# Kernel optimization log

Hardware: AMD Instinct MI355X
Metric: run time of the kernel (lower is better)

## Reference

```python
import jax, jax.numpy as jnp
import numpy as np

N_NODES = 100000
N_EDGES = 1600000
D_IN = 256
N_HEADS = 4
D_OUT = 32
NEG_SLOPE = 0.2


def setup_inputs() -> dict:
    key = jax.random.key(0)
    k1, k2, k3, k4, k5, k6 = jax.random.split(key, 6)
    x = jax.random.normal(k1, (N_NODES, D_IN), dtype=jnp.float32)
    fc_w = jax.random.normal(k2, (N_HEADS * D_OUT, D_IN), dtype=jnp.float32) * (1.0 / np.sqrt(D_IN))
    attn_l = jax.random.normal(k3, (N_HEADS, D_OUT), dtype=jnp.float32) * 0.1
    attn_r = jax.random.normal(k4, (N_HEADS, D_OUT), dtype=jnp.float32) * 0.1
    src = jax.random.randint(k5, (N_EDGES,), 0, N_NODES, dtype=jnp.int64)
    dst = jax.random.randint(k6, (N_EDGES,), 0, N_NODES, dtype=jnp.int64)
    return {"x": x, "fc_w": fc_w, "attn_l": attn_l, "attn_r": attn_r, "src": src, "dst": dst}


def reference(x, fc_w, attn_l, attn_r, src, dst):
    N = x.shape[0]
    H, F = attn_l.shape
    # Linear projection: ft = fc(x) viewed as [N, H, F]
    ft = (x @ fc_w.T).reshape(N, H, F)
    # Per-node attention logits: el = <ft, a_l>, er = <ft, a_r>  -> [N, H]
    el = jnp.einsum("nhf,hf->nh", ft, attn_l)
    er = jnp.einsum("nhf,hf->nh", ft, attn_r)
    # Edge scores: e = leaky_relu(el[src] + er[dst])  -> [E, H]
    e = el[src] + er[dst]
    e = jnp.where(e > 0, e, NEG_SLOPE * e)
    # Segment (per-destination-node) softmax over incoming edges
    m = jax.ops.segment_max(e, dst, num_segments=N)  # [N, H]
    ex = jnp.exp(e - m[dst])                          # [E, H]
    denom = jax.ops.segment_sum(ex, dst, num_segments=N)  # [N, H]
    a = ex / denom[dst]                               # [E, H]
    # Weighted scatter-sum aggregation: out[n] = sum_{e: dst=n} a_e * ft[src_e]
    out = jax.ops.segment_sum(ft[src] * a[:, :, None], dst, num_segments=N)  # [N, H, F]
    return out
```

## Files before the change

### kernel.cpp

```cpp
#include <hip/hip_runtime.h>
#include <math.h>

#define N_NODES 100000
#define N_EDGES 1600000
#define D_IN 256
#define N_HEADS 4
#define D_OUT 32
#define D_HID 128
#define NEG_SLOPE 0.2f

#define BUCKET_SHIFT 8
#define BUCKET_NODES 256
#define NB ((N_NODES + BUCKET_NODES - 1) / BUCKET_NODES)
#define CAP 6144
#define TILE 2048
#define EPT 8
#define N_TILES ((N_EDGES + TILE - 1) / TILE)

typedef __attribute__((ext_vector_type(8))) short bf16x8;
typedef __attribute__((ext_vector_type(4))) float f32x4;

static __device__ __forceinline__ unsigned cvt2(float lo, float hi) {
  unsigned r;
  asm("v_cvt_pk_bf16_f32 %0, %1, %2" : "=v"(r) : "v"(lo), "v"(hi));
  return r;
}
static __device__ __forceinline__ float bfu_lo(unsigned u) {
  union { unsigned u; float f; } c; c.u = u << 16; return c.f;
}
static __device__ __forceinline__ float bfu_hi(unsigned u) {
  union { unsigned u; float f; } c; c.u = u & 0xFFFF0000u; return c.f;
}

__global__ __launch_bounds__(256) void k_wcvt(const float* __restrict__ w,
                                              unsigned short* __restrict__ wb) {
  int i = blockIdx.x * 256 + threadIdx.x;
  if (i < (D_HID * D_IN) / 4) {
    float4 v = ((const float4*)w)[i];
    ((uint2*)wb)[i] = make_uint2(cvt2(v.x, v.y), cvt2(v.z, v.w));
  }
}

__global__ __launch_bounds__(256, 1) void k_gemm(const float* __restrict__ x,
                                                 const unsigned short* __restrict__ wb,
                                                 const float* __restrict__ al,
                                                 const float* __restrict__ ar,
                                                 unsigned short* __restrict__ ftb,
                                                 float* __restrict__ el,
                                                 float* __restrict__ er) {
  __shared__ char lds[131072];
  char* As = lds;
  char* Ws = lds + 65536;
  int t = threadIdx.x;
  int wave = t >> 6, lane = t & 63;
  int quad = lane >> 4, l16 = lane & 15;
  int rowBlk = blockIdx.x * 128;

  {
    int r = t >> 1, h = t & 1;
    int grow = rowBlk + r;
    bool v = grow < N_NODES;
    const float* xp = x + (size_t)(v ? grow : 0) * D_IN + h * 128;
    unsigned swz = (unsigned)((r & 7) << 4);
    char* abase = As + r * 512 + h * 256;
    char* wbase = Ws + r * 512 + h * 256;
    const uint4* wp = (const uint4*)wb + t * 16;
    const float4 z4 = make_float4(0.f, 0.f, 0.f, 0.f);
    #pragma unroll
    for (int c = 0; c < 16; ++c) {
      float4 v0 = v ? *(const float4*)(xp + c * 8) : z4;
      float4 v1 = v ? *(const float4*)(xp + c * 8 + 4) : z4;
      uint4 wv = wp[c];
      uint4 av = make_uint4(cvt2(v0.x, v0.y), cvt2(v0.z, v0.w),
                            cvt2(v1.x, v1.y), cvt2(v1.z, v1.w));
      *(uint4*)(abase + ((unsigned)(c * 16) ^ swz)) = av;
      *(uint4*)(wbase + ((unsigned)(c * 16) ^ swz)) = wv;
    }
  }
  __syncthreads();

  f32x4 acc[2][8];
  #pragma unroll
  for (int mt = 0; mt < 2; ++mt)
    #pragma unroll
    for (int nt = 0; nt < 8; ++nt) {
      acc[mt][nt][0] = 0.f; acc[mt][nt][1] = 0.f;
      acc[mt][nt][2] = 0.f; acc[mt][nt][3] = 0.f;
    }
  unsigned swzL = (unsigned)((l16 & 7) << 4);
  int m0 = wave * 32 + l16;
  #pragma unroll
  for (int kb = 0; kb < 8; ++kb) {
    unsigned ko = (unsigned)(kb * 64 + quad * 16);
    bf16x8 a0 = *(const bf16x8*)(As + m0 * 512 + (ko ^ swzL));
    bf16x8 a1 = *(const bf16x8*)(As + (m0 + 16) * 512 + (ko ^ swzL));
    bf16x8 b[8];
    #pragma unroll
    for (int nt = 0; nt < 8; ++nt)
      b[nt] = *(const bf16x8*)(Ws + (nt * 16 + l16) * 512 + (ko ^ swzL));
    #pragma unroll
    for (int nt = 0; nt < 8; ++nt) {
      acc[0][nt] = __builtin_amdgcn_mfma_f32_16x16x32_bf16(a0, b[nt], acc[0][nt], 0, 0, 0);
      acc[1][nt] = __builtin_amdgcn_mfma_f32_16x16x32_bf16(a1, b[nt], acc[1][nt], 0, 0, 0);
    }
  }

  int rowBase = rowBlk + wave * 32;

  #pragma unroll
  for (int mt = 0; mt < 2; ++mt) {
    #pragma unroll
    for (int nt = 0; nt < 8; ++nt) {
      int col = nt * 16 + l16;
      #pragma unroll
      for (int r = 0; r < 4; r += 2) {
        unsigned p = cvt2(acc[mt][nt][r], acc[mt][nt][r + 1]);
        int row = rowBase + mt * 16 + quad * 4 + r;
        if (row < N_NODES)
          ftb[(size_t)row * D_HID + col] = (unsigned short)p;
        if (row + 1 < N_NODES)
          ftb[(size_t)(row + 1) * D_HID + col] = (unsigned short)(p >> 16);
      }
    }
  }

  float alf[8], arf[8];
  #pragma unroll
  for (int nt = 0; nt < 8; ++nt) {
    alf[nt] = al[nt * 16 + l16];
    arf[nt] = ar[nt * 16 + l16];
  }
  #pragma unroll
  for (int mt = 0; mt < 2; ++mt) {
    #pragma unroll
    for (int r = 0; r < 4; ++r) {
      int row = rowBase + mt * 16 + quad * 4 + r;
      float sl[4], sr[4];
      #pragma unroll
      for (int h = 0; h < 4; ++h) {
        sl[h] = acc[mt][2 * h][r] * alf[2 * h] + acc[mt][2 * h + 1][r] * alf[2 * h + 1];
        sr[h] = acc[mt][2 * h][r] * arf[2 * h] + acc[mt][2 * h + 1][r] * arf[2 * h + 1];
      }
      #pragma unroll
      for (int o = 1; o < 16; o <<= 1) {
        #pragma unroll
        for (int h = 0; h < 4; ++h) {
          sl[h] += __shfl_xor(sl[h], o);
          sr[h] += __shfl_xor(sr[h], o);
        }
      }
      if (l16 == 0 && row < N_NODES) {
        *(float4*)&el[row * 4] = make_float4(sl[0], sl[1], sl[2], sl[3]);
        *(float4*)&er[row * 4] = make_float4(sr[0], sr[1], sr[2], sr[3]);
      }
    }
  }
}

__global__ __launch_bounds__(256) void k_bucket(const int* __restrict__ src,
                                                const int* __restrict__ dst,
                                                int* __restrict__ gfill,
                                                unsigned* __restrict__ pairs,
                                                int* __restrict__ offs) {
  __shared__ int bcnt[NB];
  __shared__ int brsv[NB];
  __shared__ int brank[NB];
  int t = threadIdx.x;
  if (blockIdx.x == 0 && t == 0) offs[N_NODES] = N_EDGES;
  for (int tile = blockIdx.x; tile < N_TILES; tile += gridDim.x) {
    int e0 = tile * TILE + t * EPT;
    for (int i = t; i < NB; i += 256) { bcnt[i] = 0; brank[i] = 0; }
    __syncthreads();
    int ds[EPT], ss[EPT];
    if (e0 + EPT <= N_EDGES) {
      *(int4*)&ds[0] = *(const int4*)&dst[e0];
      *(int4*)&ds[4] = *(const int4*)&dst[e0 + 4];
      *(int4*)&ss[0] = *(const int4*)&src[e0];
      *(int4*)&ss[4] = *(const int4*)&src[e0 + 4];
    } else {
      #pragma unroll
      for (int k = 0; k < EPT; ++k) {
        int e = e0 + k;
        ds[k] = (e < N_EDGES) ? dst[e] : -1;
        ss[k] = (e < N_EDGES) ? src[e] : 0;
      }
    }
    #pragma unroll
    for (int k = 0; k < EPT; ++k)
      if (ds[k] >= 0) atomicAdd(&bcnt[ds[k] >> BUCKET_SHIFT], 1);
    __syncthreads();
    for (int i = t; i < NB; i += 256) {
      int c = bcnt[i];
      brsv[i] = (c > 0) ? atomicAdd(&gfill[i], c) : 0;
    }
    __syncthreads();
    #pragma unroll
    for (int k = 0; k < EPT; ++k) {
      if (ds[k] >= 0) {
        int b = ds[k] >> BUCKET_SHIFT;
        int r = brsv[b] + atomicAdd(&brank[b], 1);
        if (r < CAP)
          pairs[(size_t)b * CAP + r] =
              ((unsigned)ss[k] << 8) | (unsigned)(ds[k] & (BUCKET_NODES - 1));
      }
    }
    __syncthreads();
  }
}

__global__ __launch_bounds__(512) void k_localsort(const unsigned* __restrict__ pairs,
                                                   const int* __restrict__ gfill,
                                                   int* __restrict__ offs,
                                                   int* __restrict__ ssrc) {
  __shared__ int cnt_l[256];
  __shared__ int ss[256];
  __shared__ int cur_l[256];
  __shared__ int redsum[8];
  __shared__ int s_base;
  int b = blockIdx.x, t = threadIdx.x;
  {
    int v = (t < NB && t < b) ? gfill[t] : 0;
    #pragma unroll
    for (int o = 32; o > 0; o >>= 1) v += __shfl_xor(v, o);
    if ((t & 63) == 0) redsum[t >> 6] = v;
  }
  if (t < 256) cnt_l[t] = 0;
  __syncthreads();
  if (t == 0) {
    int s = 0;
    #pragma unroll
    for (int i = 0; i < 8; ++i) s += redsum[i];
    s_base = s;
  }
  int E = min(gfill[b], CAP);
  const unsigned* pb = &pairs[(size_t)b * CAP];
  __syncthreads();
  int base = s_base;
  for (int i = t; i < E; i += 512)
    atomicAdd(&cnt_l[pb[i] & (BUCKET_NODES - 1)], 1);
  __syncthreads();
  if (t < 256) ss[t] = cnt_l[t];
  __syncthreads();
  #pragma unroll
  for (int d = 1; d < 256; d <<= 1) {
    int u = (t < 256 && t >= d) ? ss[t - d] : 0;
    __syncthreads();
    if (t < 256) ss[t] += u;
    __syncthreads();
  }
  if (t < 256) {
    int pre = (t == 0) ? 0 : ss[t - 1];
    int node = b * BUCKET_NODES + t;
    if (node < N_NODES) offs[node] = base + pre;
    cur_l[t] = pre;
  }
  __syncthreads();
  for (int i = t; i < E; i += 512) {
    unsigned p = pb[i];
    int pos = atomicAdd(&cur_l[p & (BUCKET_NODES - 1)], 1);
    ssrc[base + pos] = (int)(p >> 8);
  }
}

#define AH_PAD 36
__global__ __launch_bounds__(256) void k_agg(const int* __restrict__ offs,
                                             const int* __restrict__ ssrc,
                                             const unsigned short* __restrict__ ftb,
                                             const float* __restrict__ el,
                                             const float* __restrict__ er,
                                             float* __restrict__ out) {
  __shared__ int   lds_s[4][2][32];
  __shared__ float lds_ah[4][2][4][AH_PAD];
  int wave = threadIdx.x >> 6;
  int lane = threadIdx.x & 63;
  int half = lane >> 5;
  int l32 = lane & 31;
  int n = blockIdx.x * 8 + wave * 2 + half;
  if (n >= N_NODES) return;
  int start = offs[n], end = offs[n + 1];
  int deg = end - start;

  int* sS = lds_s[wave][half];
  float (*sA)[AH_PAD] = lds_ah[wave][half];

  int c4 = l32 * 4;
  int hh = l32 >> 3;
  const unsigned short* fb = ftb + c4;
  float a0 = 0.f, a1 = 0.f, a2 = 0.f, a3 = 0.f;

  float4 er4 = *(const float4*)&er[n * 4];

  if (deg <= 32) {
    bool valid = l32 < deg;
    int s = valid ? ssrc[start + l32] : 0;
    float4 e4 = *(const float4*)&el[s * 4];
    float v[4] = {e4.x + er4.x, e4.y + er4.y, e4.z + er4.z, e4.w + er4.w};
    float m[4], ex[4], den[4];
    #pragma unroll
    for (int h = 0; h < 4; ++h) {
      v[h] = v[h] > 0.f ? v[h] : NEG_SLOPE * v[h];
      m[h] = valid ? v[h] : -INFINITY;
    }
    #pragma unroll
    for (int h = 0; h < 4; ++h)
      #pragma unroll
      for (int o = 16; o > 0; o >>= 1) m[h] = fmaxf(m[h], __shfl_xor(m[h], o));
    #pragma unroll
    for (int h = 0; h < 4; ++h) {
      ex[h] = valid ? __expf(v[h] - m[h]) : 0.f;
      den[h] = ex[h];
    }
    #pragma unroll
    for (int h = 0; h < 4; ++h)
      #pragma unroll
      for (int o = 16; o > 0; o >>= 1) den[h] += __shfl_xor(den[h], o);
    sS[l32] = s;
    #pragma unroll
    for (int h = 0; h < 4; ++h) sA[h][l32] = ex[h] / den[h];
    __builtin_amdgcn_wave_barrier();
    for (int j = 0; j < deg; j += 4) {
      int4   sv = *(const int4*)&sS[j];
      float4 av = *(const float4*)&sA[hh][j];
      uint2 uA = *(const uint2*)&fb[(size_t)sv.x * D_HID];
      uint2 uB = *(const uint2*)&fb[(size_t)sv.y * D_HID];
      uint2 uC = *(const uint2*)&fb[(size_t)sv.z * D_HID];
      uint2 uD = *(const uint2*)&fb[(size_t)sv.w * D_HID];
      a0 += av.x * bfu_lo(uA.x); a1 += av.x * bfu_hi(uA.x);
      a2 += av.x * bfu_lo(uA.y); a3 += av.x * bfu_hi(uA.y);
      a0 += av.y * bfu_lo(uB.x); a1 += av.y * bfu_hi(uB.x);
      a2 += av.y * bfu_lo(uB.y); a3 += av.y * bfu_hi(uB.y);
      a0 += av.z * bfu_lo(uC.x); a1 += av.z * bfu_hi(uC.x);
      a2 += av.z * bfu_lo(uC.y); a3 += av.z * bfu_hi(uC.y);
      a0 += av.w * bfu_lo(uD.x); a1 += av.w * bfu_hi(uD.x);
      a2 += av.w * bfu_lo(uD.y); a3 += av.w * bfu_hi(uD.y);
    }
  } else {
    float erh[4] = {er4.x, er4.y, er4.z, er4.w};
    float m[4] = {-INFINITY, -INFINITY, -INFINITY, -INFINITY};
    for (int c = start; c < end; c += 32) {
      int i = c + l32;
      bool valid = i < end;
      int s = valid ? ssrc[i] : 0;
      float4 e4 = *(const float4*)&el[s * 4];
      float ee[4] = {e4.x, e4.y, e4.z, e4.w};
      #pragma unroll
      for (int h = 0; h < 4; ++h) {
        float v = ee[h] + erh[h];
        v = v > 0.f ? v : NEG_SLOPE * v;
        m[h] = fmaxf(m[h], valid ? v : -INFINITY);
      }
    }
    #pragma unroll
    for (int h = 0; h < 4; ++h)
      #pragma unroll
      for (int o = 16; o > 0; o >>= 1) m[h] = fmaxf(m[h], __shfl_xor(m[h], o));
    float den[4] = {0.f, 0.f, 0.f, 0.f};
    for (int c = start; c < end; c += 32) {
      int i = c + l32;
      bool valid = i < end;
      int s = valid ? ssrc[i] : 0;
      float4 e4 = *(const float4*)&el[s * 4];
      float ee[4] = {e4.x, e4.y, e4.z, e4.w};
      #pragma unroll
      for (int h = 0; h < 4; ++h) {
        float v = ee[h] + erh[h];
        v = v > 0.f ? v : NEG_SLOPE * v;
        den[h] += valid ? __expf(v - m[h]) : 0.f;
      }
    }
    #pragma unroll
    for (int h = 0; h < 4; ++h)
      #pragma unroll
      for (int o = 16; o > 0; o >>= 1) den[h] += __shfl_xor(den[h], o);
    float invd[4];
    #pragma unroll
    for (int h = 0; h < 4; ++h) invd[h] = 1.f / den[h];
    for (int c = start; c < end; c += 32) {
      int i = c + l32;
      bool valid = i < end;
      int s = valid ? ssrc[i] : 0;
      float4 e4 = *(const float4*)&el[s * 4];
      float ee[4] = {e4.x, e4.y, e4.z, e4.w};
      float av[4];
      #pragma unroll
      for (int h = 0; h < 4; ++h) {
        float v = ee[h] + erh[h];
        v = v > 0.f ? v : NEG_SLOPE * v;
        av[h] = valid ? __expf(v - m[h]) * invd[h] : 0.f;
      }
      __builtin_amdgcn_wave_barrier();
      sS[l32] = s;
      #pragma unroll
      for (int h = 0; h < 4; ++h) sA[h][l32] = av[h];
      __builtin_amdgcn_wave_barrier();
      int cnt = min(32, end - c);
      for (int j = 0; j < cnt; j += 4) {
        int4   sv = *(const int4*)&sS[j];
        float4 aw = *(const float4*)&sA[hh][j];
        uint2 uA = *(const uint2*)&fb[(size_t)sv.x * D_HID];
        uint2 uB = *(const uint2*)&fb[(size_t)sv.y * D_HID];
        uint2 uC = *(const uint2*)&fb[(size_t)sv.z * D_HID];
        uint2 uD = *(const uint2*)&fb[(size_t)sv.w * D_HID];
        a0 += aw.x * bfu_lo(uA.x); a1 += aw.x * bfu_hi(uA.x);
        a2 += aw.x * bfu_lo(uA.y); a3 += aw.x * bfu_hi(uA.y);
        a0 += aw.y * bfu_lo(uB.x); a1 += aw.y * bfu_hi(uB.x);
        a2 += aw.y * bfu_lo(uB.y); a3 += aw.y * bfu_hi(uB.y);
        a0 += aw.z * bfu_lo(uC.x); a1 += aw.z * bfu_hi(uC.x);
        a2 += aw.z * bfu_lo(uC.y); a3 += aw.z * bfu_hi(uC.y);
        a0 += aw.w * bfu_lo(uD.x); a1 += aw.w * bfu_hi(uD.x);
        a2 += aw.w * bfu_lo(uD.y); a3 += aw.w * bfu_hi(uD.y);
      }
    }
  }
  *(float4*)&out[(size_t)n * D_HID + c4] = make_float4(a0, a1, a2, a3);
}

extern "C" void kernel_launch(void* const* d_in, const int* in_sizes, int n_in,
                              void* d_out, int out_size, void* d_ws, size_t ws_size,
                              hipStream_t stream) {
  const float* x      = (const float*)d_in[0];
  const float* fc_w   = (const float*)d_in[1];
  const float* attn_l = (const float*)d_in[2];
  const float* attn_r = (const float*)d_in[3];
  const int*   src    = (const int*)d_in[4];
  const int*   dst    = (const int*)d_in[5];
  float* out = (float*)d_out;

  char* wsp = (char*)d_ws;
  size_t off = 0;
  auto alloc = [&](size_t bytes) {
    void* p = wsp + off;
    off = (off + bytes + 255) & ~(size_t)255;
    return p;
  };
  unsigned short* ftb = (unsigned short*)alloc((size_t)N_NODES * D_HID * 2);
  unsigned short* wb  = (unsigned short*)alloc((size_t)D_HID * D_IN * 2);
  float* el     = (float*)alloc((size_t)N_NODES * 4 * 4);
  float* er     = (float*)alloc((size_t)N_NODES * 4 * 4);
  int*   offs   = (int*)alloc((size_t)(N_NODES + 1) * 4);
  int*   ssrc   = (int*)alloc((size_t)N_EDGES * 4);
  int*   gfill  = (int*)alloc((size_t)NB * 4);
  unsigned* pairs = (unsigned*)alloc((size_t)NB * CAP * 4);

  hipMemsetAsync(gfill, 0, (size_t)NB * 4, stream);
  k_wcvt<<<(D_HID * D_IN / 4 + 255) / 256, 256, 0, stream>>>(fc_w, wb);
  k_gemm<<<(N_NODES + 127) / 128, 256, 0, stream>>>(x, wb, attn_l, attn_r, ftb, el, er);
  k_bucket<<<N_TILES, 256, 0, stream>>>(src, dst, gfill, pairs, offs);
  k_localsort<<<NB, 512, 0, stream>>>(pairs, gfill, offs, ssrc);
  k_agg<<<(N_NODES + 7) / 8, 256, 0, stream>>>(offs, ssrc, ftb, el, er, out);
}
```

Measured before the change: 366.3 us.

## Double-buffer GEMM K-loop with direct global-to-LDS async loads

Result: faster. 313.7 us (-14.4%).

```diff
diff --git a/kernel.cpp b/kernel.cpp
--- a/kernel.cpp
+++ b/kernel.cpp
@@ -32,6 +32,11 @@
   union { unsigned u; float f; } c; c.u = u & 0xFFFF0000u; return c.f;
 }
 
+#define GL2LDS(g, l) \
+  __builtin_amdgcn_global_load_lds( \
+      (const __attribute__((address_space(1))) unsigned*)(g), \
+      (__attribute__((address_space(3))) unsigned*)(l), 16, 0, 0)
+
 __global__ __launch_bounds__(256) void k_wcvt(const float* __restrict__ w,
                                               unsigned short* __restrict__ wb) {
   int i = blockIdx.x * 256 + threadIdx.x;
@@ -41,43 +46,24 @@
   }
 }
 
-__global__ __launch_bounds__(256, 1) void k_gemm(const float* __restrict__ x,
-                                                 const unsigned short* __restrict__ wb,
-                                                 const float* __restrict__ al,
-                                                 const float* __restrict__ ar,
-                                                 unsigned short* __restrict__ ftb,
-                                                 float* __restrict__ el,
-                                                 float* __restrict__ er) {
-  __shared__ char lds[131072];
-  char* As = lds;
-  char* Ws = lds + 65536;
+__global__ __launch_bounds__(256) void k_gemm(const float* __restrict__ x,
+                                              const unsigned short* __restrict__ wb,
+                                              const float* __restrict__ al,
+                                              const float* __restrict__ ar,
+                                              unsigned short* __restrict__ ftb,
+                                              float* __restrict__ el,
+                                              float* __restrict__ er) {
+  __shared__ uint4 AsU[2][1024];
+  __shared__ uint4 BsU[2][512];
   int t = threadIdx.x;
   int wave = t >> 6, lane = t & 63;
   int quad = lane >> 4, l16 = lane & 15;
   int rowBlk = blockIdx.x * 128;
 
-  {
-    int r = t >> 1, h = t & 1;
-    int grow = rowBlk + r;
-    bool v = grow < N_NODES;
-    const float* xp = x + (size_t)(v ? grow : 0) * D_IN + h * 128;
-    unsigned swz = (unsigned)((r & 7) << 4);
-    char* abase = As + r * 512 + h * 256;
-    char* wbase = Ws + r * 512 + h * 256;
-    const uint4* wp = (const uint4*)wb + t * 16;
-    const float4 z4 = make_float4(0.f, 0.f, 0.f, 0.f);
-    #pragma unroll
-    for (int c = 0; c < 16; ++c) {
-      float4 v0 = v ? *(const float4*)(xp + c * 8) : z4;
-      float4 v1 = v ? *(const float4*)(xp + c * 8 + 4) : z4;
-      uint4 wv = wp[c];
-      uint4 av = make_uint4(cvt2(v0.x, v0.y), cvt2(v0.z, v0.w),
-                            cvt2(v1.x, v1.y), cvt2(v1.z, v1.w));
-      *(uint4*)(abase + ((unsigned)(c * 16) ^ swz)) = av;
-      *(uint4*)(wbase + ((unsigned)(c * 16) ^ swz)) = wv;
-    }
-  }
-  __syncthreads();
+  int arowL = wave * 32 + (lane >> 3);
+  int aswz  = ((lane & 7) ^ (lane >> 3)) * 16;
+  int browL = wave * 32 + (lane >> 2);
+  int brem  = (lane & 3) * 16;
 
   f32x4 acc[2][8];
   #pragma unroll
@@ -87,23 +73,60 @@
       acc[mt][nt][0] = 0.f; acc[mt][nt][1] = 0.f;
       acc[mt][nt][2] = 0.f; acc[mt][nt][3] = 0.f;
     }
-  unsigned swzL = (unsigned)((l16 & 7) << 4);
-  int m0 = wave * 32 + l16;
-  #pragma unroll
-  for (int kb = 0; kb < 8; ++kb) {
-    unsigned ko = (unsigned)(kb * 64 + quad * 16);
-    bf16x8 a0 = *(const bf16x8*)(As + m0 * 512 + (ko ^ swzL));
-    bf16x8 a1 = *(const bf16x8*)(As + (m0 + 16) * 512 + (ko ^ swzL));
-    bf16x8 b[8];
+
+  const char* xB  = (const char*)x;
+  const char* wbB = (const char*)wb;
+
+  #define STAGE(buf, tt) do {                                              \
+    int kA = (tt) * 128;                                                   \
+    int kB = (tt) * 64;                                                    \
+    _Pragma("unroll")                                                      \
+    for (int i = 0; i < 4; ++i) {                                          \
+      int grow = rowBlk + arowL + i * 8;                                   \
+      if (grow >= N_NODES) grow = N_NODES - 1;                             \
+      GL2LDS(xB + (size_t)grow * 1024 + kA + aswz,                         \
+             (char*)&AsU[buf][0] + wave * 4096 + i * 1024);                \
+    }                                                                      \
+    _Pragma("unroll")                                                      \
+    for (int i = 0; i < 2; ++i) {                                          \
+      int brw = browL + i * 16;                                            \
+      GL2LDS(wbB + (size_t)brw * 512 + kB + brem,                          \
+             (char*)&BsU[buf][0] + wave * 2048 + i * 1024);                \
+    }                                                                      \
+  } while (0)
+
+  STAGE(0, 0);
+  __syncthreads();
+
+  int rA = wave * 32 + l16;
+  int sA = l16 & 7;
+  #pragma unroll
+  for (int tt = 0; tt < 8; ++tt) {
+    int cur = tt & 1;
+    if (tt < 7) STAGE(cur ^ 1, tt + 1);
+    const char* Ab = (const char*)&AsU[cur][0];
+    const char* Bb = (const char*)&BsU[cur][0];
+    float4 fa00 = *(const float4*)(Ab + rA * 128 + (((quad * 2)     ^ sA) << 4));
+    float4 fa01 = *(const float4*)(Ab + rA * 128 + (((quad * 2 + 1) ^ sA) << 4));
+    float4 fa10 = *(const float4*)(Ab + (rA + 16) * 128 + (((quad * 2)     ^ sA) << 4));
+    float4 fa11 = *(const float4*)(Ab + (rA + 16) * 128 + (((quad * 2 + 1) ^ sA) << 4));
+    bf16x8 bfr[8];
     #pragma unroll
     for (int nt = 0; nt < 8; ++nt)
-      b[nt] = *(const bf16x8*)(Ws + (nt * 16 + l16) * 512 + (ko ^ swzL));
+      bfr[nt] = *(const bf16x8*)(Bb + (nt * 16 + l16) * 64 + quad * 16);
+    union { unsigned u[4]; bf16x8 v; } a0c, a1c;
+    a0c.u[0] = cvt2(fa00.x, fa00.y); a0c.u[1] = cvt2(fa00.z, fa00.w);
+    a0c.u[2] = cvt2(fa01.x, fa01.y); a0c.u[3] = cvt2(fa01.z, fa01.w);
+    a1c.u[0] = cvt2(fa10.x, fa10.y); a1c.u[1] = cvt2(fa10.z, fa10.w);
+    a1c.u[2] = cvt2(fa11.x, fa11.y); a1c.u[3] = cvt2(fa11.z, fa11.w);
     #pragma unroll
     for (int nt = 0; nt < 8; ++nt) {
-      acc[0][nt] = __builtin_amdgcn_mfma_f32_16x16x32_bf16(a0, b[nt], acc[0][nt], 0, 0, 0);
-      acc[1][nt] = __builtin_amdgcn_mfma_f32_16x16x32_bf16(a1, b[nt], acc[1][nt], 0, 0, 0);
-    }
-  }
+      acc[0][nt] = __builtin_amdgcn_mfma_f32_16x16x32_bf16(a0c.v, bfr[nt], acc[0][nt], 0, 0, 0);
+      acc[1][nt] = __builtin_amdgcn_mfma_f32_16x16x32_bf16(a1c.v, bfr[nt], acc[1][nt], 0, 0, 0);
+    }
+    __syncthreads();
+  }
+  #undef STAGE
 
   int rowBase = rowBlk + wave * 32;
 
```
